# Kernel optimization log

Measured on AMD Instinct MI355X. Metric: run time of the kernel, lower is better.

The kernel has to match this reference:

```python
import jax, jax.numpy as jnp
import numpy as np

TAG = 64
START = 0
END = 1
NEG = -10000.0


def setup_inputs() -> dict:
    key = jax.random.key(0)
    kf, kw, kl = jax.random.split(key, 3)
    B, T, K = 1024, 512, TAG
    feats = jax.random.normal(kf, (B, T, K), dtype=jnp.float32)
    w = jax.random.uniform(kw, (K, K), minval=-1.0 / K, maxval=1.0 / K, dtype=jnp.float32)
    # default adjacency: forbid transitions into start (row START) and out of end (col END)
    adj = jnp.zeros((K, K), jnp.float32).at[START, :].set(1.0).at[:, END].set(1.0)
    weights = w + NEG * adj
    lens = jax.random.randint(kl, (B,), 1, T + 1)  # 1..T inclusive
    return {"feats": feats, "weights": weights, "lens": lens}


def reference(feats, weights, lens):
    # feats: [B, T, K], weights: [K, K] with weights[next, prev], lens: [B]
    B, T, K = feats.shape
    init = jnp.full((B, K), NEG, feats.dtype).at[:, START].set(0.0)
    mask_tb = (jnp.arange(T)[None, :] < lens[:, None]).T  # [T, B]
    ident = jnp.arange(K, dtype=jnp.int32)

    def step(fv, inp):
        feat, m = inp  # feat: [B, K], m: [B]
        scores = fv[:, None, :] + weights[None, :, :]  # [B, next, prev]
        new_fv = jnp.max(scores, axis=-1) + feat       # emission added after max
        bptr = jnp.argmax(scores, axis=-1).astype(jnp.int32)
        fv2 = jnp.where(m[:, None], new_fv, fv)
        bptr2 = jnp.where(m[:, None], bptr, ident[None, :])  # identity keeps backtrace valid past len
        return fv2, bptr2

    fv, bptrs = jax.lax.scan(step, init, (jnp.swapaxes(feats, 0, 1), mask_tb))
    terminal = fv + weights[END][None, :]              # transition to end tag
    best_last = jnp.argmax(terminal, axis=-1)
    path_score = jnp.take_along_axis(terminal, best_last[:, None], axis=1)[:, 0]

    def back(tag, bp):  # tag: [B], bp: [B, K]
        prev = jnp.take_along_axis(bp, tag[:, None], axis=1)[:, 0]
        return prev, tag  # emit tag chosen at this timestep

    _, path = jax.lax.scan(back, best_last.astype(jnp.int32), bptrs, reverse=True)
    best_paths = jnp.swapaxes(path, 0, 1)  # [B, T]; positions >= lens[b] are padding
    return path_score, best_paths
```

## Files before the change

### kernel.cpp

```cpp
#include <hip/hip_runtime.h>

#define TAGS 64
#define MAXT 512
#define NEG  -10000.0f
#define CH   8

__global__ __launch_bounds__(64, 1) void crf_viterbi(
    const float* __restrict__ feats,
    const float* __restrict__ weights,
    const int*   __restrict__ lens,
    float*       __restrict__ out,
    int B, int T)
{
    const int b    = blockIdx.x;
    const int lane = threadIdx.x;
    const int len  = lens[b];

    __shared__ float fv[TAGS];
    __shared__ float fbuf[2][CH * TAGS];
    __shared__ unsigned char  bptr[MAXT * TAGS];
    __shared__ unsigned short path[MAXT];

    float w[TAGS];
    #pragma unroll
    for (int i = 0; i < 16; ++i) {
        const float4 v = *reinterpret_cast<const float4*>(weights + lane * TAGS + i * 4);
        w[4*i+0] = v.x; w[4*i+1] = v.y; w[4*i+2] = v.z; w[4*i+3] = v.w;
    }
    const float wEnd = weights[1 * TAGS + lane];

    fv[lane] = (lane == 0) ? 0.0f : NEG;

    const float* fb  = feats + (size_t)b * T * TAGS;
    const int    lim = len * TAGS - 4;

    float nf = NEG;
    auto step = [&](int cbuf, int i, int t) {
        const float feat = fbuf[cbuf][i * TAGS + lane];
        float gv[16]; int gi[16];
        #pragma unroll
        for (int g = 0; g < 16; ++g) {
            const float4 fq = *reinterpret_cast<const float4*>(&fv[g * 4]);
            const float c0 = fq.x + w[4*g+0];
            const float c1 = fq.y + w[4*g+1];
            const float c2 = fq.z + w[4*g+2];
            const float c3 = fq.w + w[4*g+3];
            const bool g01 = c1 > c0;
            const float v01 = g01 ? c1 : c0; const int i01 = g01 ? (4*g+1) : (4*g+0);
            const bool g23 = c3 > c2;
            const float v23 = g23 ? c3 : c2; const int i23 = g23 ? (4*g+3) : (4*g+2);
            const bool gg = v23 > v01;
            gv[g] = gg ? v23 : v01; gi[g] = gg ? i23 : i01;
        }
        #pragma unroll
        for (int n = 8; n >= 1; n >>= 1) {
            #pragma unroll
            for (int k = 0; k < n; ++k) {
                const bool g = gv[2*k+1] > gv[2*k];
                gv[k] = g ? gv[2*k+1] : gv[2*k];
                gi[k] = g ? gi[2*k+1] : gi[2*k];
            }
        }
        nf = gv[0] + feat;
        fv[lane] = nf;
        bptr[t * TAGS + lane] = (unsigned char)gi[0];
    };

    {
        int o0 = 4 * lane;        if (o0 > lim) o0 = lim;
        int o1 = 256 + 4 * lane;  if (o1 > lim) o1 = lim;
        const float4 r0 = *reinterpret_cast<const float4*>(fb + o0);
        const float4 r1 = *reinterpret_cast<const float4*>(fb + o1);
        *reinterpret_cast<float4*>(&fbuf[0][4 * lane])       = r0;
        *reinterpret_cast<float4*>(&fbuf[0][256 + 4 * lane]) = r1;
    }
    float4 n0, n1;
    {
        int o0 = CH * TAGS + 4 * lane;        if (o0 > lim) o0 = lim;
        int o1 = CH * TAGS + 256 + 4 * lane;  if (o1 > lim) o1 = lim;
        n0 = *reinterpret_cast<const float4*>(fb + o0);
        n1 = *reinterpret_cast<const float4*>(fb + o1);
    }

    int cb = 0;
    const int nfull = len / CH;
    for (int c = 0; c < nfull; ++c) {
        #pragma unroll
        for (int i = 0; i < CH; ++i) step(cb, i, c * CH + i);
        *reinterpret_cast<float4*>(&fbuf[cb ^ 1][4 * lane])       = n0;
        *reinterpret_cast<float4*>(&fbuf[cb ^ 1][256 + 4 * lane]) = n1;
        {
            int o0 = (c + 2) * CH * TAGS + 4 * lane;        if (o0 > lim) o0 = lim;
            int o1 = (c + 2) * CH * TAGS + 256 + 4 * lane;  if (o1 > lim) o1 = lim;
            n0 = *reinterpret_cast<const float4*>(fb + o0);
            n1 = *reinterpret_cast<const float4*>(fb + o1);
        }
        cb ^= 1;
    }
    const int rem = len - nfull * CH;
    for (int i = 0; i < rem; ++i) step(cb, i, nfull * CH + i);

    float tv = nf + wEnd;
    int   ti = lane;
    #pragma unroll
    for (int off = 32; off >= 1; off >>= 1) {
        const float ov = __shfl_xor(tv, off);
        const int   oi = __shfl_xor(ti, off);
        if (ov > tv || (ov == tv && oi < ti)) { tv = ov; ti = oi; }
    }
    if (lane == 0) out[b] = tv;
    const int bestlast = ti;

    for (int t = lane; t < T; t += 64)
        if (t >= len - 1) path[t] = (unsigned short)bestlast;
    __builtin_amdgcn_wave_barrier();

    if (lane == 0) {
        int tag = bestlast;
        for (int t = len - 1; t >= 1; --t) {
            tag = bptr[t * TAGS + tag];
            path[t - 1] = (unsigned short)tag;
        }
    }
    __builtin_amdgcn_wave_barrier();

    float* pout = out + B + (size_t)b * T;
    for (int t = lane; t < T; t += 64)
        pout[t] = (float)path[t];
}

extern "C" void kernel_launch(void* const* d_in, const int* in_sizes, int n_in,
                              void* d_out, int out_size, void* d_ws, size_t ws_size,
                              hipStream_t stream) {
    const float* feats   = (const float*)d_in[0];
    const float* weights = (const float*)d_in[1];
    const int*   lens    = (const int*)d_in[2];
    float*       out     = (float*)d_out;

    const int B = in_sizes[2];
    const int T = in_sizes[0] / (B * TAGS);

    crf_viterbi<<<dim3(B), dim3(64), 0, stream>>>(feats, weights, lens, out, B, T);
}
```

Baseline: 435.2 us.

## Split Viterbi max over previous tags across two waves per sequence

Each block now runs two waves that each handle half of the previous-tag candidates for every next tag. Wave 1 passes its partial max and argmax through shared memory, and wave 0 merges them, adds the emission and writes the forward value and backpointer. This halves the serial compare chain each wave runs per timestep, which should shorten the latency-bound recurrence. The cost is two block-wide barriers and an extra shared-memory round trip per step, plus twice the waves competing for each CU.

New measurement: 468.4 us. 1.08x slower.

```diff
diff --git a/kernel.cpp b/kernel.cpp
--- a/kernel.cpp
+++ b/kernel.cpp
@@ -5,7 +5,7 @@
 #define NEG  -10000.0f
 #define CH   8
 
-__global__ __launch_bounds__(64, 1) void crf_viterbi(
+__global__ __launch_bounds__(128, 1) void crf_viterbi(
     const float* __restrict__ feats,
     const float* __restrict__ weights,
     const int*   __restrict__ lens,
@@ -13,47 +13,66 @@
     int B, int T)
 {
     const int b    = blockIdx.x;
-    const int lane = threadIdx.x;
+    const int tid  = threadIdx.x;
+    const int lane = tid & 63;
+    const int wv   = tid >> 6;
     const int len  = lens[b];
 
-    __shared__ float fv[TAGS];
-    __shared__ float fbuf[2][CH * TAGS];
+    __shared__ float  fv[TAGS];
+    __shared__ float2 part[TAGS];
+    __shared__ float  fbuf[2][CH * TAGS];
     __shared__ unsigned char  bptr[MAXT * TAGS];
     __shared__ unsigned short path[MAXT];
+    __shared__ int s_best;
 
-    float w[TAGS];
+    float w[32];
     #pragma unroll
-    for (int i = 0; i < 16; ++i) {
-        const float4 v = *reinterpret_cast<const float4*>(weights + lane * TAGS + i * 4);
+    for (int i = 0; i < 8; ++i) {
+        const float4 v = *reinterpret_cast<const float4*>(
+            weights + lane * TAGS + wv * 32 + i * 4);
         w[4*i+0] = v.x; w[4*i+1] = v.y; w[4*i+2] = v.z; w[4*i+3] = v.w;
     }
     const float wEnd = weights[1 * TAGS + lane];
 
-    fv[lane] = (lane == 0) ? 0.0f : NEG;
+    if (wv == 0) fv[lane] = (lane == 0) ? 0.0f : NEG;
 
     const float* fb  = feats + (size_t)b * T * TAGS;
     const int    lim = len * TAGS - 4;
 
+    float4 n0, n1;
+    if (wv == 0) {
+        int o0 = 4 * lane;        if (o0 > lim) o0 = lim;
+        int o1 = 256 + 4 * lane;  if (o1 > lim) o1 = lim;
+        *reinterpret_cast<float4*>(&fbuf[0][4 * lane])       = *reinterpret_cast<const float4*>(fb + o0);
+        *reinterpret_cast<float4*>(&fbuf[0][256 + 4 * lane]) = *reinterpret_cast<const float4*>(fb + o1);
+        int p0 = CH * TAGS + 4 * lane;        if (p0 > lim) p0 = lim;
+        int p1 = CH * TAGS + 256 + 4 * lane;  if (p1 > lim) p1 = lim;
+        n0 = *reinterpret_cast<const float4*>(fb + p0);
+        n1 = *reinterpret_cast<const float4*>(fb + p1);
+    }
+    __syncthreads();
+
     float nf = NEG;
+
     auto step = [&](int cbuf, int i, int t) {
-        const float feat = fbuf[cbuf][i * TAGS + lane];
-        float gv[16]; int gi[16];
+        float gv[8]; int gi[8];
         #pragma unroll
-        for (int g = 0; g < 16; ++g) {
-            const float4 fq = *reinterpret_cast<const float4*>(&fv[g * 4]);
+        for (int g = 0; g < 8; ++g) {
+            const float4 fq = *reinterpret_cast<const float4*>(&fv[wv * 32 + g * 4]);
+            const int base = wv * 32 + g * 4;
             const float c0 = fq.x + w[4*g+0];
             const float c1 = fq.y + w[4*g+1];
             const float c2 = fq.z + w[4*g+2];
             const float c3 = fq.w + w[4*g+3];
             const bool g01 = c1 > c0;
-            const float v01 = g01 ? c1 : c0; const int i01 = g01 ? (4*g+1) : (4*g+0);
+            const float v01 = g01 ? c1 : c0; const int i01 = base + (g01 ? 1 : 0);
             const bool g23 = c3 > c2;
-            const float v23 = g23 ? c3 : c2; const int i23 = g23 ? (4*g+3) : (4*g+2);
+            const float v23 = g23 ? c3 : c2; const int i23 = base + (g23 ? 3 : 2);
             const bool gg = v23 > v01;
             gv[g] = gg ? v23 : v01; gi[g] = gg ? i23 : i01;
         }
         #pragma unroll
-        for (int n = 8; n >= 1; n >>= 1) {
+        for (int n = 4; n >= 1; n >>= 1) {
             #pragma unroll
             for (int k = 0; k < n; ++k) {
                 const bool g = gv[2*k+1] > gv[2*k];
@@ -61,71 +80,70 @@
                 gi[k] = g ? gi[2*k+1] : gi[2*k];
             }
         }
-        nf = gv[0] + feat;
-        fv[lane] = nf;
-        bptr[t * TAGS + lane] = (unsigned char)gi[0];
+        float feat = 0.0f;
+        if (wv == 1) {
+            float2 p; p.x = gv[0]; p.y = __int_as_float(gi[0]);
+            part[lane] = p;
+        } else {
+            feat = fbuf[cbuf][i * TAGS + lane];
+        }
+        __syncthreads();
+        if (wv == 0) {
+            const float2 p = part[lane];
+            const bool g = p.x > gv[0];
+            const float val = g ? p.x : gv[0];
+            const int   idx = g ? __float_as_int(p.y) : gi[0];
+            nf = val + feat;
+            fv[lane] = nf;
+            bptr[t * TAGS + lane] = (unsigned char)idx;
+        }
+        __syncthreads();
     };
 
-    {
-        int o0 = 4 * lane;        if (o0 > lim) o0 = lim;
-        int o1 = 256 + 4 * lane;  if (o1 > lim) o1 = lim;
-        const float4 r0 = *reinterpret_cast<const float4*>(fb + o0);
-        const float4 r1 = *reinterpret_cast<const float4*>(fb + o1);
-        *reinterpret_cast<float4*>(&fbuf[0][4 * lane])       = r0;
-        *reinterpret_cast<float4*>(&fbuf[0][256 + 4 * lane]) = r1;
-    }
-    float4 n0, n1;
-    {
-        int o0 = CH * TAGS + 4 * lane;        if (o0 > lim) o0 = lim;
-        int o1 = CH * TAGS + 256 + 4 * lane;  if (o1 > lim) o1 = lim;
-        n0 = *reinterpret_cast<const float4*>(fb + o0);
-        n1 = *reinterpret_cast<const float4*>(fb + o1);
-    }
-
-    int cb = 0;
     const int nfull = len / CH;
     for (int c = 0; c < nfull; ++c) {
         #pragma unroll
-        for (int i = 0; i < CH; ++i) step(cb, i, c * CH + i);
-        *reinterpret_cast<float4*>(&fbuf[cb ^ 1][4 * lane])       = n0;
-        *reinterpret_cast<float4*>(&fbuf[cb ^ 1][256 + 4 * lane]) = n1;
-        {
+        for (int i = 0; i < CH; ++i) step(c & 1, i, c * CH + i);
+        if (wv == 0) {
+            *reinterpret_cast<float4*>(&fbuf[(c + 1) & 1][4 * lane])       = n0;
+            *reinterpret_cast<float4*>(&fbuf[(c + 1) & 1][256 + 4 * lane]) = n1;
             int o0 = (c + 2) * CH * TAGS + 4 * lane;        if (o0 > lim) o0 = lim;
             int o1 = (c + 2) * CH * TAGS + 256 + 4 * lane;  if (o1 > lim) o1 = lim;
             n0 = *reinterpret_cast<const float4*>(fb + o0);
             n1 = *reinterpret_cast<const float4*>(fb + o1);
         }
-        cb ^= 1;
     }
     const int rem = len - nfull * CH;
-    for (int i = 0; i < rem; ++i) step(cb, i, nfull * CH + i);
+    for (int i = 0; i < rem; ++i) step(nfull & 1, i, nfull * CH + i);
 
-    float tv = nf + wEnd;
-    int   ti = lane;
-    #pragma unroll
-    for (int off = 32; off >= 1; off >>= 1) {
-        const float ov = __shfl_xor(tv, off);
-        const int   oi = __shfl_xor(ti, off);
-        if (ov > tv || (ov == tv && oi < ti)) { tv = ov; ti = oi; }
+    if (wv == 0) {
+        float tv = nf + wEnd;
+        int   ti = lane;
+        #pragma unroll
+        for (int off = 32; off >= 1; off >>= 1) {
+            const float ov = __shfl_xor(tv, off);
+            const int   oi = __shfl_xor(ti, off);
+            if (ov > tv || (ov == tv && oi < ti)) { tv = ov; ti = oi; }
+        }
+        if (lane == 0) { out[b] = tv; s_best = ti; }
     }
-    if (lane == 0) out[b] = tv;
-    const int bestlast = ti;
+    __syncthreads();
+    const int bestlast = s_best;
 
-    for (int t = lane; t < T; t += 64)
+    for (int t = tid; t < T; t += 128)
         if (t >= len - 1) path[t] = (unsigned short)bestlast;
-    __builtin_amdgcn_wave_barrier();
 
-    if (lane == 0) {
+    if (tid == 0) {
         int tag = bestlast;
         for (int t = len - 1; t >= 1; --t) {
             tag = bptr[t * TAGS + tag];
             path[t - 1] = (unsigned short)tag;
         }
     }
-    __builtin_amdgcn_wave_barrier();
+    __syncthreads();
 
     float* pout = out + B + (size_t)b * T;
-    for (int t = lane; t < T; t += 64)
+    for (int t = tid; t < T; t += 128)
         pout[t] = (float)path[t];
 }
 
@@ -140,5 +158,5 @@
     const int B = in_sizes[2];
     const int T = in_sizes[0] / (B * TAGS);
 
-    crf_viterbi<<<dim3(B), dim3(64), 0, stream>>>(feats, weights, lens, out, B, T);
+    crf_viterbi<<<dim3(B), dim3(128), 0, stream>>>(feats, weights, lens, out, B, T);
 }
```
